# Kernel tuning notes

Hardware: AMD Instinct MI355X
Metric: run time of the kernel (lower is better)

The kernel has to match this reference:

```python
import jax, jax.numpy as jnp
import numpy as np
from jax import lax

BATCH = 4096
SEQ = 200
VOCAB = 100000
HID = 128


def setup_inputs() -> dict:
    key = jax.random.key(0)
    k0, k1, k2, k3, k4 = jax.random.split(key, 5)
    inputs = jax.random.randint(k0, (BATCH, SEQ), 0, VOCAB, dtype=jnp.int32).astype(jnp.int64)
    emb = jax.random.normal(k1, (VOCAB, HID), dtype=jnp.float32) * 0.05
    # Keras GRU (reset_after=True): kernel [H,3H], recurrent_kernel [H,3H], bias [2,3H]
    kernel = jax.random.normal(k2, (HID, 3 * HID), dtype=jnp.float32) * (1.0 / np.sqrt(HID))
    rec_kernel = jax.random.normal(k3, (HID, 3 * HID), dtype=jnp.float32) * (1.0 / np.sqrt(HID))
    bias = jax.random.normal(k4, (2, 3 * HID), dtype=jnp.float32) * 0.01
    return {"inputs": inputs, "emb": emb, "kernel": kernel, "rec_kernel": rec_kernel, "bias": bias}


def _masked_gru(x, mask, kernel, rec_kernel, bias):
    # x: [B,S,H] embedded inputs; mask: [B,S] bool (True = valid timestep)
    input_bias, rec_bias = bias[0], bias[1]
    # Precompute all input projections in one big GEMM: [B,S,3H]
    xproj = jnp.einsum('bsh,hk->bsk', x, kernel) + input_bias
    B, H = x.shape[0], x.shape[2]

    def step(h, scan_in):
        xp, m = scan_in  # xp: [B,3H], m: [B]
        hp = h @ rec_kernel + rec_bias  # [B,3H]
        xz, xr, xh = xp[:, :H], xp[:, H:2 * H], xp[:, 2 * H:]
        hz, hr, hh_rec = hp[:, :H], hp[:, H:2 * H], hp[:, 2 * H:]
        z = jax.nn.sigmoid(xz + hz)
        r = jax.nn.sigmoid(xr + hr)
        hh = jnp.tanh(xh + r * hh_rec)  # reset_after=True: r applied after recurrent matmul
        h_new = z * h + (1.0 - z) * hh
        # mask_zero semantics: masked steps carry previous state through
        h_new = jnp.where(m[:, None], h_new, h)
        return h_new, None

    h0 = jnp.zeros((B, H), dtype=x.dtype)
    xs = (jnp.swapaxes(xproj, 0, 1), jnp.swapaxes(mask, 0, 1))  # time-major
    h_final, _ = lax.scan(step, h0, xs)
    return h_final  # [B,H] == last valid-step output under Keras masking


def reference(inputs, emb, kernel, rec_kernel, bias):
    x = emb[inputs]              # [B,S,H] embedding lookup
    mask = inputs != 0           # mask_zero=True
    return _masked_gru(x, mask, kernel, rec_kernel, bias)
```

## Files before the change

### kernel.cpp

```cpp
#include <hip/hip_runtime.h>

#define BATCH 4096
#define SEQ   200
#define HID   128
#define ROWS  16
#define NTH   512

typedef _Float16 f16;
typedef f16 f16x4 __attribute__((ext_vector_type(4)));
typedef f16 f16x8 __attribute__((ext_vector_type(8)));
typedef float f32x4 __attribute__((ext_vector_type(4)));

#define MFMA(a, b, c) __builtin_amdgcn_mfma_f32_16x16x32_f16((a), (b), (c), 0, 0, 0)

__device__ __forceinline__ float fast_exp2(float x) {
#if defined(__has_builtin) && __has_builtin(__builtin_amdgcn_exp2f)
    return __builtin_amdgcn_exp2f(x);
#else
    float r; asm volatile("v_exp_f32 %0, %1\n\ts_nop 0" : "=v"(r) : "v"(x)); return r;
#endif
}
__device__ __forceinline__ float fast_rcp(float x) {
#if defined(__has_builtin) && __has_builtin(__builtin_amdgcn_rcpf)
    return __builtin_amdgcn_rcpf(x);
#else
    float r; asm volatile("v_rcp_f32 %0, %1\n\ts_nop 0" : "=v"(r) : "v"(x)); return r;
#endif
}
#define LOG2E  1.442695041f
#define LOG2E2 2.885390082f

__global__ __attribute__((amdgpu_flat_work_group_size(NTH, NTH)))
void gru_mfma(const int* __restrict__ inputs,
              const float* __restrict__ emb,
              const float* __restrict__ kernel,
              const float* __restrict__ rec_kernel,
              const float* __restrict__ bias,
              float* __restrict__ out)
{
    __shared__ __align__(16) f16 xb[2][4][64][8];
    __shared__ __align__(16) f16 hb[2][4][64][8];
    __shared__ int tok_sh[2][ROWS];
    __shared__ int ts_sh;

    const int tid  = threadIdx.x;
    const int lane = tid & 63;
    const int j0   = (tid >> 6) * 16;
    const int l15  = lane & 15;
    const int hi   = lane >> 4;
    const int r0   = hi * 4;
    const int row0 = blockIdx.x * ROWS;

    if (tid == 0) { int any = 0; for (int i = 1; i < 128; i += 2) any |= inputs[i]; ts_sh = any ? 1 : 2; }

    f16x8 Bx[3][4];
    f16x8 Brz[4], Brr[4], Brh[4];
    const float gsc[3] = { -LOG2E, -LOG2E, LOG2E2 };
#pragma unroll
    for (int g = 0; g < 3; ++g)
#pragma unroll
        for (int kt = 0; kt < 4; ++kt) {
            f16x8 t;
#pragma unroll
            for (int e = 0; e < 8; ++e)
                t[e] = (f16)(gsc[g] * kernel[(size_t)(kt * 32 + hi * 8 + e) * 384 + g * HID + j0 + l15]);
            Bx[g][kt] = t;
        }
#pragma unroll
    for (int kt = 0; kt < 4; ++kt) {
        f16x8 tz, tr, th;
#pragma unroll
        for (int e = 0; e < 8; ++e) {
            const size_t krow = (size_t)(kt * 32 + hi * 8 + e) * 384;
            tz[e] = (f16)(-LOG2E  * rec_kernel[krow + j0 + l15]);
            tr[e] = (f16)(-LOG2E  * rec_kernel[krow + HID + j0 + l15]);
            th[e] = (f16)(LOG2E2 * rec_kernel[krow + 2 * HID + j0 + l15]);
        }
        Brz[kt] = tz; Brr[kt] = tr; Brh[kt] = th;
    }

    f32x4 bzv, brv, bxhv, brhv;
#pragma unroll
    for (int i = 0; i < 4; ++i) {
        const int c = j0 + r0 + i;
        bzv[i]  = -LOG2E * (bias[c]       + bias[384 + c]);
        brv[i]  = -LOG2E * (bias[128 + c] + bias[512 + c]);
        bxhv[i] =  LOG2E2 * bias[256 + c];
        brhv[i] =  LOG2E2 * bias[640 + c];
    }

    f32x4 h = {0.f, 0.f, 0.f, 0.f};

    const int hk  = j0 + r0;
    const int hwi = (((hk >> 5) * 64) + (((hk & 31) >> 3) * 16) + l15) * 8 + (hk & 7);

    const int rr = tid >> 5;
    const int c4 = (tid & 31) * 4;
    const int xwi = (((c4 >> 5) * 64) + (((c4 & 31) >> 3) * 16) + rr) * 8 + (c4 & 7);

    for (int i = tid; i < 4 * 64 * 8; i += NTH) ((f16*)hb)[i] = (f16)0.f;
    __syncthreads();
    const int ts = ts_sh;

    {
        const int tok0 = inputs[((size_t)(row0 + rr) * SEQ + 0) * ts];
        if ((tid & 31) == 0) tok_sh[0][rr] = tok0;
        const float4 ev = *(const float4*)&emb[(size_t)tok0 * HID + c4];
        f16x4 xv; xv[0] = (f16)ev.x; xv[1] = (f16)ev.y; xv[2] = (f16)ev.z; xv[3] = (f16)ev.w;
        *(f16x4*)&((f16*)xb)[xwi] = xv;
    }
    int tokA = inputs[((size_t)(row0 + rr) * SEQ + 1) * ts];
    __syncthreads();

    for (int s = 0; s < SEQ; ++s) {
        const int cur = s & 1, nxt = cur ^ 1;
        const bool pf = (s + 1 < SEQ);
        float4 ev; int tokB = tokA;
        if (pf) {
            ev = *(const float4*)&emb[(size_t)tokA * HID + c4];
            const int s2 = (s + 2 < SEQ) ? (s + 2) : (SEQ - 1);
            tokB = inputs[((size_t)(row0 + rr) * SEQ + s2) * ts];
        }

        const int tkk = tok_sh[cur][l15];

        f32x4 azx = bzv, arx = brv, ax = bxhv;
        f32x4 azh = {0.f, 0.f, 0.f, 0.f}, arh = {0.f, 0.f, 0.f, 0.f};
        f32x4 ah  = brhv;
#pragma unroll
        for (int kt = 0; kt < 4; ++kt) {
            const f16x8 xB = *(const f16x8*)&xb[cur][kt][lane][0];
            const f16x8 hB = *(const f16x8*)&hb[cur][kt][lane][0];
            azx = MFMA(Bx[0][kt], xB, azx);
            arx = MFMA(Bx[1][kt], xB, arx);
            ax  = MFMA(Bx[2][kt], xB, ax);
            azh = MFMA(Brz[kt], hB, azh);
            arh = MFMA(Brr[kt], hB, arh);
            ah  = MFMA(Brh[kt], hB, ah);
        }

        f16x4 hv;
#pragma unroll
        for (int i = 0; i < 4; ++i) {
            const float z  = fast_rcp(1.f + fast_exp2(azx[i] + azh[i]));
            const float rg = fast_rcp(1.f + fast_exp2(arx[i] + arh[i]));
            const float u  = ax[i] + rg * ah[i];
            const float hh = 1.f - 2.f * fast_rcp(1.f + fast_exp2(u));
            const float hn = hh + z * (h[i] - hh);
            h[i] = (tkk != 0) ? hn : h[i];
            hv[i] = (f16)h[i];
        }

        *(f16x4*)&((f16*)hb)[nxt * (4 * 64 * 8) + hwi] = hv;
        if (pf) {
            f16x4 xv; xv[0] = (f16)ev.x; xv[1] = (f16)ev.y; xv[2] = (f16)ev.z; xv[3] = (f16)ev.w;
            *(f16x4*)&((f16*)xb)[nxt * (4 * 64 * 8) + xwi] = xv;
            if ((tid & 31) == 0) tok_sh[nxt][rr] = tokA;
            tokA = tokB;
        }
        __syncthreads();
    }

    float4 o; o.x = h[0]; o.y = h[1]; o.z = h[2]; o.w = h[3];
    *(float4*)&out[(size_t)(row0 + l15) * HID + j0 + r0] = o;
}

extern "C" void kernel_launch(void* const* d_in, const int* in_sizes, int n_in,
                              void* d_out, int out_size, void* d_ws, size_t ws_size,
                              hipStream_t stream) {
    const int* inputs      = (const int*)d_in[0];
    const float* emb       = (const float*)d_in[1];
    const float* kernel    = (const float*)d_in[2];
    const float* rec_k     = (const float*)d_in[3];
    const float* bias      = (const float*)d_in[4];
    float* out             = (float*)d_out;
    gru_mfma<<<BATCH / ROWS, NTH, 0, stream>>>(inputs, emb, kernel, rec_k, bias, out);
}
```

Before: 173.1 us.

## Software-pipeline input projection one step ahead of the recurrent MFMA chain

Moves the input-projection MFMAs for step s+1 after the hidden-state update of step s, so the serial critical path per step is only the recurrent matmul and gate math. Token mask values are now prefetched per lane into registers three steps ahead, replacing the shared tok_sh array. The embedding staging layout is remapped so each thread writes a matching 4-element chunk. The loop is manually unrolled by two with compile-time buffer indices. This adds register pressure and a deeper prefetch pipeline.

```diff
diff --git a/kernel.cpp b/kernel.cpp
--- a/kernel.cpp
+++ b/kernel.cpp
@@ -5,6 +5,7 @@
 #define HID   128
 #define ROWS  16
 #define NTH   512
+#define FB    (4 * 64 * 8)
 
 typedef _Float16 f16;
 typedef f16 f16x4 __attribute__((ext_vector_type(4)));
@@ -40,7 +41,6 @@
 {
     __shared__ __align__(16) f16 xb[2][4][64][8];
     __shared__ __align__(16) f16 hb[2][4][64][8];
-    __shared__ int tok_sh[2][ROWS];
     __shared__ int ts_sh;
 
     const int tid  = threadIdx.x;
@@ -94,72 +94,95 @@
     const int hk  = j0 + r0;
     const int hwi = (((hk >> 5) * 64) + (((hk & 31) >> 3) * 16) + l15) * 8 + (hk & 7);
 
-    const int rr = tid >> 5;
-    const int c4 = (tid & 31) * 4;
-    const int xwi = (((c4 >> 5) * 64) + (((c4 & 31) >> 3) * 16) + rr) * 8 + (c4 & 7);
-
-    for (int i = tid; i < 4 * 64 * 8; i += NTH) ((f16*)hb)[i] = (f16)0.f;
+    const int skt   = tid >> 7;
+    const int sidx  = tid & 127;
+    const int su    = sidx >> 1;
+    const int shalf = sidx & 1;
+    const int sb    = su & 15;
+    const int shid  = skt * 32 + (su >> 4) * 8 + shalf * 4;
+    const int sw    = (skt * 64 + su) * 8 + shalf * 4;
+
+    for (int i = tid; i < FB; i += NTH) ((f16*)hb)[i] = (f16)0.f;
     __syncthreads();
     const int ts = ts_sh;
 
+    const size_t tbS = (size_t)(row0 + sb)  * SEQ;
+    const size_t tbG = (size_t)(row0 + l15) * SEQ;
+    int gA = inputs[(tbG + 0) * ts];
+    int gB = inputs[(tbG + 1) * ts];
+    int gC = inputs[(tbG + 2) * ts];
+    const int tk0 = inputs[(tbS + 0) * ts];
+    const int tk1 = inputs[(tbS + 1) * ts];
+    int tok2 = inputs[(tbS + 2) * ts];
+
     {
-        const int tok0 = inputs[((size_t)(row0 + rr) * SEQ + 0) * ts];
-        if ((tid & 31) == 0) tok_sh[0][rr] = tok0;
-        const float4 ev = *(const float4*)&emb[(size_t)tok0 * HID + c4];
-        f16x4 xv; xv[0] = (f16)ev.x; xv[1] = (f16)ev.y; xv[2] = (f16)ev.z; xv[3] = (f16)ev.w;
-        *(f16x4*)&((f16*)xb)[xwi] = xv;
-    }
-    int tokA = inputs[((size_t)(row0 + rr) * SEQ + 1) * ts];
+        const float4 v0 = *(const float4*)&emb[(size_t)tk0 * HID + shid];
+        const float4 v1 = *(const float4*)&emb[(size_t)tk1 * HID + shid];
+        f16x4 a; a[0] = (f16)v0.x; a[1] = (f16)v0.y; a[2] = (f16)v0.z; a[3] = (f16)v0.w;
+        f16x4 b; b[0] = (f16)v1.x; b[1] = (f16)v1.y; b[2] = (f16)v1.z; b[3] = (f16)v1.w;
+        *(f16x4*)&((f16*)xb)[sw] = a;
+        *(f16x4*)&((f16*)xb)[FB + sw] = b;
+    }
     __syncthreads();
 
-    for (int s = 0; s < SEQ; ++s) {
-        const int cur = s & 1, nxt = cur ^ 1;
-        const bool pf = (s + 1 < SEQ);
-        float4 ev; int tokB = tokA;
-        if (pf) {
-            ev = *(const float4*)&emb[(size_t)tokA * HID + c4];
-            const int s2 = (s + 2 < SEQ) ? (s + 2) : (SEQ - 1);
-            tokB = inputs[((size_t)(row0 + rr) * SEQ + s2) * ts];
-        }
-
-        const int tkk = tok_sh[cur][l15];
-
-        f32x4 azx = bzv, arx = brv, ax = bxhv;
-        f32x4 azh = {0.f, 0.f, 0.f, 0.f}, arh = {0.f, 0.f, 0.f, 0.f};
-        f32x4 ah  = brhv;
-#pragma unroll
-        for (int kt = 0; kt < 4; ++kt) {
-            const f16x8 xB = *(const f16x8*)&xb[cur][kt][lane][0];
-            const f16x8 hB = *(const f16x8*)&hb[cur][kt][lane][0];
-            azx = MFMA(Bx[0][kt], xB, azx);
-            arx = MFMA(Bx[1][kt], xB, arx);
-            ax  = MFMA(Bx[2][kt], xB, ax);
-            azh = MFMA(Brz[kt], hB, azh);
-            arh = MFMA(Brr[kt], hB, arh);
-            ah  = MFMA(Brh[kt], hB, ah);
-        }
-
-        f16x4 hv;
-#pragma unroll
-        for (int i = 0; i < 4; ++i) {
-            const float z  = fast_rcp(1.f + fast_exp2(azx[i] + azh[i]));
-            const float rg = fast_rcp(1.f + fast_exp2(arx[i] + arh[i]));
-            const float u  = ax[i] + rg * ah[i];
-            const float hh = 1.f - 2.f * fast_rcp(1.f + fast_exp2(u));
-            const float hn = hh + z * (h[i] - hh);
-            h[i] = (tkk != 0) ? hn : h[i];
-            hv[i] = (f16)h[i];
-        }
-
-        *(f16x4*)&((f16*)hb)[nxt * (4 * 64 * 8) + hwi] = hv;
-        if (pf) {
-            f16x4 xv; xv[0] = (f16)ev.x; xv[1] = (f16)ev.y; xv[2] = (f16)ev.z; xv[3] = (f16)ev.w;
-            *(f16x4*)&((f16*)xb)[nxt * (4 * 64 * 8) + xwi] = xv;
-            if ((tid & 31) == 0) tok_sh[nxt][rr] = tokA;
-            tokA = tokB;
-        }
-        __syncthreads();
-    }
+    f32x4 azx = bzv, arx = brv, axc = bxhv;
+#pragma unroll
+    for (int kt = 0; kt < 4; ++kt) {
+        const f16x8 xB = *(const f16x8*)&xb[0][kt][lane][0];
+        azx = MFMA(Bx[0][kt], xB, azx);
+        arx = MFMA(Bx[1][kt], xB, arx);
+        axc = MFMA(Bx[2][kt], xB, axc);
+    }
+
+#define GRU_STEP(HRD, HWR, XRD, XWR, SOFF)                                     \
+    {                                                                          \
+        const int sl = (ss + (SOFF) < SEQ) ? ss + (SOFF) : SEQ - 1;            \
+        const float4 pv = *(const float4*)&emb[(size_t)tok2 * HID + shid];     \
+        const int tokN = inputs[(tbS + sl) * ts];                              \
+        const int gN   = inputs[(tbG + sl) * ts];                              \
+        f32x4 az = azx, ar = arx, ah = brhv;                                   \
+        _Pragma("unroll")                                                      \
+        for (int kt = 0; kt < 4; ++kt) {                                       \
+            const f16x8 hB = *(const f16x8*)&hb[HRD][kt][lane][0];             \
+            az = MFMA(Brz[kt], hB, az);                                        \
+            ar = MFMA(Brr[kt], hB, ar);                                        \
+            ah = MFMA(Brh[kt], hB, ah);                                        \
+        }                                                                      \
+        f16x4 hv;                                                              \
+        _Pragma("unroll")                                                      \
+        for (int i = 0; i < 4; ++i) {                                          \
+            const float z  = fast_rcp(1.f + fast_exp2(az[i]));                 \
+            const float rg = fast_rcp(1.f + fast_exp2(ar[i]));                 \
+            const float u  = axc[i] + rg * ah[i];                              \
+            const float hh = 1.f - 2.f * fast_rcp(1.f + fast_exp2(u));         \
+            const float hn = hh + z * (h[i] - hh);                             \
+            h[i] = (gA != 0) ? hn : h[i];                                      \
+            hv[i] = (f16)h[i];                                                 \
+        }                                                                      \
+        *(f16x4*)&((f16*)hb)[(HWR) * FB + hwi] = hv;                           \
+                      \
+        azx = bzv; arx = brv; axc = bxhv;                                      \
+        _Pragma("unroll")                                                      \
+        for (int kt = 0; kt < 4; ++kt) {                                       \
+            const f16x8 xB = *(const f16x8*)&xb[XRD][kt][lane][0];             \
+            azx = MFMA(Bx[0][kt], xB, azx);                                    \
+            arx = MFMA(Bx[1][kt], xB, arx);                                    \
+            axc = MFMA(Bx[2][kt], xB, axc);                                    \
+        }                                                                      \
+        {                                                                      \
+            f16x4 xv; xv[0] = (f16)pv.x; xv[1] = (f16)pv.y;                    \
+            xv[2] = (f16)pv.z; xv[3] = (f16)pv.w;                              \
+            *(f16x4*)&((f16*)xb)[(XWR) * FB + sw] = xv;                        \
+        }                                                                      \
+        gA = gB; gB = gC; gC = gN; tok2 = tokN;                                \
+        __syncthreads();                                                       \
+    }
+
+    for (int ss = 0; ss < SEQ; ss += 2) {
+        GRU_STEP(0, 1, 1, 0, 3)
+        GRU_STEP(1, 0, 0, 1, 4)
+    }
+#undef GRU_STEP
 
     float4 o; o.x = h[0]; o.y = h[1]; o.z = h[2]; o.w = h[3];
     *(float4*)&out[(size_t)(row0 + l15) * HID + j0 + r0] = o;
```

Measured after the change: 238.1 us. 1.38x slower.
